# Kernel tuning notes

Measured on AMD Instinct MI355X. Metric: run time of the kernel, lower is better.

## Reference

```python
import jax, jax.numpy as jnp
import numpy as np

B, H, W = 8, 352, 352

def _shift(x, dr, dc):
    # zero-filled shift: out[r, c] = x[r - dr, c - dc]; matches bmm with the
    # super-diagonal translation matrices in the original code.
    x = jnp.roll(x, (dr, dc), axis=(1, 2))
    if dr > 0:
        x = x.at[:, :dr, :].set(0.0)
    elif dr < 0:
        x = x.at[:, dr:, :].set(0.0)
    if dc > 0:
        x = x.at[:, :, :dc].set(0.0)
    elif dc < 0:
        x = x.at[:, :, dc:].set(0.0)
    return x

def _bilateral_vote(c):
    # c: [B, 8, H, W] sigmoid probabilities
    a1 = c[:, 3] * _shift(c[:, 4], 0, 1)    # right
    a2 = c[:, 4] * _shift(c[:, 3], 0, -1)   # left
    a3 = c[:, 1] * _shift(c[:, 6], 1, 0)    # bottom
    a4 = c[:, 6] * _shift(c[:, 1], -1, 0)   # up
    a5 = c[:, 2] * _shift(c[:, 5], 1, -1)   # left_bottom
    a6 = c[:, 5] * _shift(c[:, 2], -1, 1)   # right_above
    a7 = c[:, 0] * _shift(c[:, 7], 1, 1)    # right_bottom
    a8 = c[:, 7] * _shift(c[:, 0], -1, -1)  # left_above
    vote = jnp.stack([a7, a3, a5, a1, a2, a6, a4, a8], axis=1)
    return vote.mean(axis=1), vote  # glo_map [B,H,W], vote_out [B,8,H,W]

def _bce_sum(p, t):
    # torch F.binary_cross_entropy clamps log terms at -100
    logp = jnp.maximum(jnp.log(p), -100.0)
    log1mp = jnp.maximum(jnp.log1p(-p), -100.0)
    return -jnp.sum(t * logp + (1.0 - t) * log1mp)

def _bce2d_new(x, t):
    # weighted BCE-with-logits, sum reduction (bce2d_new in the source)
    pos = (t == 1).astype(x.dtype)
    neg = (t == 0).astype(x.dtype)
    num_pos, num_neg = pos.sum(), neg.sum()
    tot = num_pos + num_neg
    wts = (num_neg / tot) * pos + (1.1 * num_pos / tot) * neg
    ce = jnp.maximum(x, 0.0) - x * t + jnp.log1p(jnp.exp(-jnp.abs(x)))
    return jnp.sum(wts * ce)

def _forward(up_edge, up_sal, up_sal_f, target, con_target):
    con_f = con_target.astype(jnp.float32)
    sum_conn = con_f.sum(axis=1)  # [B,H,W]
    edge_map = ((sum_conn < 8) & (sum_conn > 0)).astype(jnp.float32)
    edge_l = sum(_bce2d_new(up_edge[i], edge_map[:, None]) for i in range(up_edge.shape[0]))

    def sal_term(logits):
        p = jax.nn.sigmoid(logits)
        glo, vote = _bilateral_vote(p)
        pmin = (1.0 - vote.min(axis=1)) * edge_map
        dec = glo * (1.0 - edge_map) + pmin
        dl = _bce_sum(dec[:, None], target)
        return dl + 0.2 * _bce_sum(vote, con_f) + 0.8 * _bce_sum(p, con_f)

    sal_l = sum(sal_term(up_sal[i]) for i in range(up_sal.shape[0]))
    sal_l = sal_l + sum(sal_term(up_sal_f[i]) for i in range(up_sal_f.shape[0]))
    loss = sal_l + edge_l
    return loss, edge_l, sal_l, loss

def setup_inputs() -> dict:
    key = jax.random.key(0)
    k1, k2, k3, k4, k5 = jax.random.split(key, 5)
    return {
        'up_edge': jax.random.normal(k1, (3, B, 1, H, W), jnp.float32),
        'up_sal': jax.random.normal(k2, (2, B, 8, H, W), jnp.float32),
        'up_sal_f': jax.random.normal(k3, (2, B, 8, H, W), jnp.float32),
        'target': jax.random.uniform(k4, (B, 1, H, W), jnp.float32),
        'con_target': jax.random.randint(k5, (B, 8, H, W), 0, 2, jnp.int32),
        'edge': 0, 'weight': 1, 'voted': 0, 'unbalance': 0,
    }

def reference(up_edge, up_sal, up_sal_f, target, con_target, edge, weight, voted, unbalance):
    # edge is overwritten inside forward; weight/voted/unbalance are unused.
    return _forward(up_edge, up_sal, up_sal_f, target, con_target)
```

## Files before the change

### kernel.cpp

```cpp
#include <hip/hip_runtime.h>
#include <math.h>

#define HH 352
#define WW 352
#define IMG (HH * WW)
#define NPIX (8 * IMG)
#define NG (NPIX / 4)
#define IMG4 (IMG / 4)
#define WB (WW / 4)
#define THREADS 256
#define GBLK (NG / THREADS)

typedef float f4 __attribute__((ext_vector_type(4)));
typedef int   i4 __attribute__((ext_vector_type(4)));

__device__ __forceinline__ float rcpf_(float x) { return __builtin_amdgcn_rcpf(x); }

__device__ __forceinline__ f4 loadu4(const float* p) {
    f4 v;
    __builtin_memcpy(&v, p, 16);
    return v;
}

__device__ __forceinline__ float wave_reduce_f(float v) {
    #pragma unroll
    for (int off = 32; off > 0; off >>= 1) v += __shfl_down(v, off, 64);
    return v;
}
__device__ __forceinline__ int wave_reduce_i(int v) {
    #pragma unroll
    for (int off = 32; off > 0; off >>= 1) v += __shfl_down(v, off, 64);
    return v;
}

__global__ void k_edge(const float* __restrict__ up_edge,
                       const int* __restrict__ con,
                       unsigned int* __restrict__ packed,
                       double* __restrict__ acc,
                       unsigned int* __restrict__ npos) {
    int g = blockIdx.x * THREADS + threadIdx.x;
    int b = g / IMG4;
    int r4 = g - b * IMG4;
    const int* cb = con + (size_t)b * 8 * IMG + 4 * (size_t)r4;

    i4 c[8];
    #pragma unroll
    for (int k = 0; k < 8; k++) c[k] = *(const i4*)(cb + (size_t)k * IMG);
    f4 x[3];
    #pragma unroll
    for (int i = 0; i < 3; i++)
        x[i] = *(const f4*)(up_edge + (size_t)i * NPIX + 4 * (size_t)g);

    unsigned int pk = 0;
    float sp = 0.0f, sn = 0.0f;
    int cnt = 0;
    #pragma unroll
    for (int j = 0; j < 4; j++) {
        int s = 0;
        unsigned int byte = 0;
        #pragma unroll
        for (int k = 0; k < 8; k++) {
            int cv = c[k][j];
            s += cv;
            byte |= ((unsigned int)cv) << k;
        }
        pk |= byte << (8 * j);
        float em = (s > 0 && s < 8) ? 1.0f : 0.0f;
        float cej = 0.0f;
        #pragma unroll
        for (int i = 0; i < 3; i++) {
            float xx = x[i][j];
            cej += fmaxf(xx, 0.0f) - xx * em + __logf(1.0f + __expf(-fabsf(xx)));
        }
        sp += em * cej;
        sn += (1.0f - em) * cej;
        cnt += (int)em;
    }
    packed[g] = pk;

    sp = wave_reduce_f(sp);
    sn = wave_reduce_f(sn);
    cnt = wave_reduce_i(cnt);

    __shared__ float smp[4], smn[4];
    __shared__ int smc[4];
    int lane = threadIdx.x & 63, wid = threadIdx.x >> 6;
    if (lane == 0) { smp[wid] = sp; smn[wid] = sn; smc[wid] = cnt; }
    __syncthreads();
    if (threadIdx.x == 0) {
        atomicAdd(acc + 0, (double)(smp[0] + smp[1] + smp[2] + smp[3]));
        atomicAdd(acc + 1, (double)(smn[0] + smn[1] + smn[2] + smn[3]));
        atomicAdd(npos, (unsigned int)(smc[0] + smc[1] + smc[2] + smc[3]));
    }
}

__global__ void k_sal(const float* __restrict__ up_sal,
                      const float* __restrict__ up_sal_f,
                      const float* __restrict__ target,
                      const unsigned int* __restrict__ packed,
                      double* __restrict__ acc) {
    int g  = blockIdx.x * THREADS + threadIdx.x;
    int s4 = blockIdx.y;
    int b  = g / IMG4;
    int r4 = g - b * IMG4;
    int h  = r4 / WB;
    int wb = r4 - h * WB;

    const float* tb = (s4 < 2) ? (up_sal + (size_t)s4 * 8 * NPIX)
                               : (up_sal_f + (size_t)(s4 - 2) * 8 * NPIX);
    const float* base = tb + (size_t)b * 8 * IMG;

    unsigned int pk = packed[g];
    f4 tgt = *(const f4*)(target + 4 * (size_t)g);

    const int drs[8] = {-1, -1, -1,  0, 0,  1, 1, 1};
    const int dcs[8] = {-1,  0,  1, -1, 1, -1, 0, 1};

    f4 xc[8], xn[8];
    float hok[8];
    #pragma unroll
    for (int k = 0; k < 8; k++) {
        xc[k] = *(const f4*)(base + (size_t)k * IMG + 4 * (size_t)r4);
        int h2 = h + drs[k];
        long off = (long)(7 - k) * IMG + (long)h2 * WW + 4 * wb + dcs[k];
        off = off < 0 ? 0 : off;
        off = off > (long)(8 * IMG - 4) ? (long)(8 * IMG - 4) : off;
        xn[k] = loadu4(base + off);
        hok[k] = ((unsigned)h2 < (unsigned)HH) ? 1.0f : 0.0f;
    }

    float local = 0.0f;
    #pragma unroll
    for (int j = 0; j < 4; j++) {
        unsigned int byte = (pk >> (8 * j)) & 0xffu;
        int s = __popc(byte);
        float em = (s > 0 && s < 8) ? 1.0f : 0.0f;

        float vsum = 0.0f, vmin = 1e30f, vb = 0.0f, pb = 0.0f;
        #pragma unroll
        for (int k = 0; k < 8; k++) {
            float okc = hok[k];
            if (dcs[k] == -1 && j == 0) okc = (wb != 0)      ? okc : 0.0f;
            if (dcs[k] ==  1 && j == 3) okc = (wb != WB - 1) ? okc : 0.0f;

            float xcv = xc[k][j];
            float xnv = xn[k][j];
            float e   = __expf(-xcv);
            float pc  = rcpf_(1.0f + e);
            float sc  = __logf(1.0f + e);
            float en  = __expf(-xnv);
            float pn  = rcpf_(1.0f + en) * okc;
            float snv = (okc != 0.0f) ? __logf(1.0f + en) : 1e30f;

            float v = pc * pn;
            vsum += v;
            vmin = fminf(vmin, v);

            float t    = (float)((byte >> k) & 1u);
            float l1mv = __logf(1.0f - v);
            float vbk  = (t != 0.0f) ? (sc + snv) : (-l1mv);
            vb += fminf(vbk, 100.0f);
            float pbk  = (t != 0.0f) ? sc : (xcv + sc);
            pb += fminf(pbk, 100.0f);
        }
        float glo = vsum * 0.125f;
        float dec = (em != 0.0f) ? (1.0f - vmin) : glo;
        float lgd  = fmaxf(__logf(dec), -100.0f);
        float lg1d = fmaxf(__logf(1.0f - dec), -100.0f);
        local += -(tgt[j] * lgd + (1.0f - tgt[j]) * lg1d) + 0.2f * vb + 0.8f * pb;
    }

    local = wave_reduce_f(local);
    __shared__ float sm[4];
    int lane = threadIdx.x & 63, wid = threadIdx.x >> 6;
    if (lane == 0) sm[wid] = local;
    __syncthreads();
    if (threadIdx.x == 0)
        atomicAdd(acc, (double)(sm[0] + sm[1] + sm[2] + sm[3]));
}

__global__ void k_final(const double* __restrict__ acc,
                        const unsigned int* __restrict__ npos,
                        float* __restrict__ out) {
    if (threadIdx.x == 0) {
        double np_  = (double)(*npos);
        double tot  = (double)NPIX;
        double nn   = tot - np_;
        double wpos = nn / tot;
        double wneg = 1.1 * np_ / tot;
        double e  = wpos * acc[0] + wneg * acc[1];
        double sl = acc[2];
        double l  = e + sl;
        out[0] = (float)l;
        out[1] = (float)e;
        out[2] = (float)sl;
        out[3] = (float)l;
    }
}

extern "C" void kernel_launch(void* const* d_in, const int* in_sizes, int n_in,
                              void* d_out, int out_size, void* d_ws, size_t ws_size,
                              hipStream_t stream) {
    const float* up_edge  = (const float*)d_in[0];
    const float* up_sal   = (const float*)d_in[1];
    const float* up_sal_f = (const float*)d_in[2];
    const float* target   = (const float*)d_in[3];
    const int*   con      = (const int*)d_in[4];
    float* out = (float*)d_out;

    double*       acc    = (double*)d_ws;
    unsigned int* npos   = (unsigned int*)((char*)d_ws + 24);
    unsigned int* packed = (unsigned int*)((char*)d_ws + 64);

    hipMemsetAsync(d_ws, 0, 64, stream);
    k_edge<<<GBLK, THREADS, 0, stream>>>(up_edge, con, packed, acc, npos);
    k_sal<<<dim3(GBLK, 4), THREADS, 0, stream>>>(up_sal, up_sal_f, target, packed, acc + 2);
    k_final<<<1, 64, 0, stream>>>(acc, npos, out);
}
```

Before: 239.8 us.

## Fuse edge and saliency kernels, recompute edge map per slice, simplify vote BCE

Merges the edge BCE kernel and the saliency kernel into a single launch with an extra grid slice for the edge term; each saliency slice recomputes the connectivity byte and edge mask from con instead of reading a packed intermediate. The vote BCE now uses one log of v or 1-v instead of separate softplus and log terms. This removes a kernel launch, the inter-kernel dependency and the packed buffer, but re-reads the full int32 con tensor in every slice, increasing memory traffic unless it stays in cache.

```diff
diff --git a/kernel.cpp b/kernel.cpp
--- a/kernel.cpp
+++ b/kernel.cpp
@@ -33,84 +33,86 @@
     return v;
 }
 
-__global__ void k_edge(const float* __restrict__ up_edge,
-                       const int* __restrict__ con,
-                       unsigned int* __restrict__ packed,
-                       double* __restrict__ acc,
-                       unsigned int* __restrict__ npos) {
+__device__ __forceinline__ void block_acc(float v, double* dst) {
+    v = wave_reduce_f(v);
+    __shared__ float sm[4];
+    int lane = threadIdx.x & 63, wid = threadIdx.x >> 6;
+    if (lane == 0) sm[wid] = v;
+    __syncthreads();
+    if (threadIdx.x == 0)
+        atomicAdd(dst, (double)(sm[0] + sm[1] + sm[2] + sm[3]));
+}
+
+__global__ __launch_bounds__(THREADS, 4) void k_main(
+        const float* __restrict__ up_edge,
+        const float* __restrict__ up_sal,
+        const float* __restrict__ up_sal_f,
+        const float* __restrict__ target,
+        const int* __restrict__ con,
+        double* __restrict__ acc,
+        unsigned int* __restrict__ npos) {
     int g = blockIdx.x * THREADS + threadIdx.x;
+    int y = blockIdx.y;
     int b = g / IMG4;
     int r4 = g - b * IMG4;
+
     const int* cb = con + (size_t)b * 8 * IMG + 4 * (size_t)r4;
-
     i4 c[8];
     #pragma unroll
     for (int k = 0; k < 8; k++) c[k] = *(const i4*)(cb + (size_t)k * IMG);
-    f4 x[3];
-    #pragma unroll
-    for (int i = 0; i < 3; i++)
-        x[i] = *(const f4*)(up_edge + (size_t)i * NPIX + 4 * (size_t)g);
-
-    unsigned int pk = 0;
-    float sp = 0.0f, sn = 0.0f;
-    int cnt = 0;
+
+    unsigned int byte_[4];
+    float em_[4];
     #pragma unroll
     for (int j = 0; j < 4; j++) {
-        int s = 0;
-        unsigned int byte = 0;
-        #pragma unroll
-        for (int k = 0; k < 8; k++) {
-            int cv = c[k][j];
-            s += cv;
-            byte |= ((unsigned int)cv) << k;
+        unsigned int by = 0; int s = 0;
+        #pragma unroll
+        for (int k = 0; k < 8; k++) { int cv = c[k][j]; s += cv; by |= ((unsigned)cv) << k; }
+        byte_[j] = by;
+        em_[j] = (s > 0 && s < 8) ? 1.0f : 0.0f;
+    }
+
+    if (y == 0) {
+        f4 x[3];
+        #pragma unroll
+        for (int i = 0; i < 3; i++)
+            x[i] = *(const f4*)(up_edge + (size_t)i * NPIX + 4 * (size_t)g);
+        float sp = 0.0f, sn = 0.0f; int cnt = 0;
+        #pragma unroll
+        for (int j = 0; j < 4; j++) {
+            float em = em_[j], ce = 0.0f;
+            #pragma unroll
+            for (int i = 0; i < 3; i++) {
+                float xx = x[i][j];
+                ce += fmaxf(xx, 0.0f) - xx * em + __logf(1.0f + __expf(-fabsf(xx)));
+            }
+            sp += em * ce;
+            sn += (1.0f - em) * ce;
+            cnt += (int)em;
         }
-        pk |= byte << (8 * j);
-        float em = (s > 0 && s < 8) ? 1.0f : 0.0f;
-        float cej = 0.0f;
-        #pragma unroll
-        for (int i = 0; i < 3; i++) {
-            float xx = x[i][j];
-            cej += fmaxf(xx, 0.0f) - xx * em + __logf(1.0f + __expf(-fabsf(xx)));
+        sp = wave_reduce_f(sp);
+        sn = wave_reduce_f(sn);
+        cnt = wave_reduce_i(cnt);
+        __shared__ float smp[4], smn[4];
+        __shared__ int smc[4];
+        int lane = threadIdx.x & 63, wid = threadIdx.x >> 6;
+        if (lane == 0) { smp[wid] = sp; smn[wid] = sn; smc[wid] = cnt; }
+        __syncthreads();
+        if (threadIdx.x == 0) {
+            atomicAdd(acc + 0, (double)(smp[0] + smp[1] + smp[2] + smp[3]));
+            atomicAdd(acc + 1, (double)(smn[0] + smn[1] + smn[2] + smn[3]));
+            atomicAdd(npos, (unsigned int)(smc[0] + smc[1] + smc[2] + smc[3]));
         }
-        sp += em * cej;
-        sn += (1.0f - em) * cej;
-        cnt += (int)em;
-    }
-    packed[g] = pk;
-
-    sp = wave_reduce_f(sp);
-    sn = wave_reduce_f(sn);
-    cnt = wave_reduce_i(cnt);
-
-    __shared__ float smp[4], smn[4];
-    __shared__ int smc[4];
-    int lane = threadIdx.x & 63, wid = threadIdx.x >> 6;
-    if (lane == 0) { smp[wid] = sp; smn[wid] = sn; smc[wid] = cnt; }
-    __syncthreads();
-    if (threadIdx.x == 0) {
-        atomicAdd(acc + 0, (double)(smp[0] + smp[1] + smp[2] + smp[3]));
-        atomicAdd(acc + 1, (double)(smn[0] + smn[1] + smn[2] + smn[3]));
-        atomicAdd(npos, (unsigned int)(smc[0] + smc[1] + smc[2] + smc[3]));
-    }
-}
-
-__global__ void k_sal(const float* __restrict__ up_sal,
-                      const float* __restrict__ up_sal_f,
-                      const float* __restrict__ target,
-                      const unsigned int* __restrict__ packed,
-                      double* __restrict__ acc) {
-    int g  = blockIdx.x * THREADS + threadIdx.x;
-    int s4 = blockIdx.y;
-    int b  = g / IMG4;
-    int r4 = g - b * IMG4;
+        return;
+    }
+
+    int s4 = y - 1;
     int h  = r4 / WB;
     int wb = r4 - h * WB;
-
     const float* tb = (s4 < 2) ? (up_sal + (size_t)s4 * 8 * NPIX)
                                : (up_sal_f + (size_t)(s4 - 2) * 8 * NPIX);
     const float* base = tb + (size_t)b * 8 * IMG;
 
-    unsigned int pk = packed[g];
     f4 tgt = *(const f4*)(target + 4 * (size_t)g);
 
     const int drs[8] = {-1, -1, -1,  0, 0,  1, 1, 1};
@@ -132,10 +134,8 @@
     float local = 0.0f;
     #pragma unroll
     for (int j = 0; j < 4; j++) {
-        unsigned int byte = (pk >> (8 * j)) & 0xffu;
-        int s = __popc(byte);
-        float em = (s > 0 && s < 8) ? 1.0f : 0.0f;
-
+        unsigned int byte = byte_[j];
+        float em = em_[j];
         float vsum = 0.0f, vmin = 1e30f, vb = 0.0f, pb = 0.0f;
         #pragma unroll
         for (int k = 0; k < 8; k++) {
@@ -144,23 +144,20 @@
             if (dcs[k] ==  1 && j == 3) okc = (wb != WB - 1) ? okc : 0.0f;
 
             float xcv = xc[k][j];
-            float xnv = xn[k][j];
             float e   = __expf(-xcv);
             float pc  = rcpf_(1.0f + e);
             float sc  = __logf(1.0f + e);
-            float en  = __expf(-xnv);
+            float en  = __expf(-xn[k][j]);
             float pn  = rcpf_(1.0f + en) * okc;
-            float snv = (okc != 0.0f) ? __logf(1.0f + en) : 1e30f;
 
             float v = pc * pn;
             vsum += v;
             vmin = fminf(vmin, v);
 
-            float t    = (float)((byte >> k) & 1u);
-            float l1mv = __logf(1.0f - v);
-            float vbk  = (t != 0.0f) ? (sc + snv) : (-l1mv);
-            vb += fminf(vbk, 100.0f);
-            float pbk  = (t != 0.0f) ? sc : (xcv + sc);
+            bool t = (byte >> k) & 1u;
+            float arg = t ? v : (1.0f - v);
+            vb += fminf(-__logf(arg), 100.0f);
+            float pbk = t ? sc : (xcv + sc);
             pb += fminf(pbk, 100.0f);
         }
         float glo = vsum * 0.125f;
@@ -169,14 +166,7 @@
         float lg1d = fmaxf(__logf(1.0f - dec), -100.0f);
         local += -(tgt[j] * lgd + (1.0f - tgt[j]) * lg1d) + 0.2f * vb + 0.8f * pb;
     }
-
-    local = wave_reduce_f(local);
-    __shared__ float sm[4];
-    int lane = threadIdx.x & 63, wid = threadIdx.x >> 6;
-    if (lane == 0) sm[wid] = local;
-    __syncthreads();
-    if (threadIdx.x == 0)
-        atomicAdd(acc, (double)(sm[0] + sm[1] + sm[2] + sm[3]));
+    block_acc(local, acc + 2);
 }
 
 __global__ void k_final(const double* __restrict__ acc,
@@ -208,12 +198,11 @@
     const int*   con      = (const int*)d_in[4];
     float* out = (float*)d_out;
 
-    double*       acc    = (double*)d_ws;
-    unsigned int* npos   = (unsigned int*)((char*)d_ws + 24);
-    unsigned int* packed = (unsigned int*)((char*)d_ws + 64);
+    double*       acc  = (double*)d_ws;
+    unsigned int* npos = (unsigned int*)((char*)d_ws + 24);
 
     hipMemsetAsync(d_ws, 0, 64, stream);
-    k_edge<<<GBLK, THREADS, 0, stream>>>(up_edge, con, packed, acc, npos);
-    k_sal<<<dim3(GBLK, 4), THREADS, 0, stream>>>(up_sal, up_sal_f, target, packed, acc + 2);
+    k_main<<<dim3(GBLK, 5), THREADS, 0, stream>>>(up_edge, up_sal, up_sal_f,
+                                                  target, con, acc, npos);
     k_final<<<1, 64, 0, stream>>>(acc, npos, out);
 }
```

Result: no change. 240.1 us (+0.1%).
